# Performance work log

Measured on AMD Instinct MI355X. Metric: run time of the kernel, lower is better.

Reference implementation:

```python
import jax, jax.numpy as jnp
import numpy as np

B, D, LP, P = 64, 256, 64, 16
N = 256                     # linear1 output = number of graph nodes (= d_model for consistent reassembly)
F = LP * P                  # per-node feature dim = SAGEConv input_dim = 1024
HID = 512                   # hidden_channels
NODE_SLICES = {"A": (0, 128), "B": (128, 192), "C": (192, 256)}
# 6 cross edge types + 3 self-loop edge types (add_self_loops=True)
EDGE_TYPES = [("A", "B"), ("B", "A"), ("A", "C"), ("C", "A"), ("B", "C"), ("C", "B"),
              ("A", "A"), ("B", "B"), ("C", "C")]
E = len(EDGE_TYPES)


def setup_inputs() -> dict:
    ks = jax.random.split(jax.random.key(0), 8)
    s = lambda fan: 1.0 / np.sqrt(fan)
    return {
        "x": jax.random.normal(ks[0], (B, D, LP, P), jnp.float32),
        "W1": jax.random.normal(ks[1], (D, N), jnp.float32) * s(D),   # linear1
        "b1": jnp.zeros((N,), jnp.float32),
        "Wl": jax.random.normal(ks[2], (E, F, HID), jnp.float32) * s(F),  # SAGEConv lin_l (aggregated msgs)
        "bl": jnp.zeros((E, HID), jnp.float32),
        "Wr": jax.random.normal(ks[3], (E, F, HID), jnp.float32) * s(F),  # SAGEConv lin_r (root, no bias)
        "Wf": jax.random.normal(ks[4], (HID, F), jnp.float32) * s(HID),   # final_linear
        "bf": jnp.zeros((F,), jnp.float32),
        "W2": jax.random.normal(ks[5], (N, D), jnp.float32) * s(N),       # linear2
        "b2": jnp.zeros((D,), jnp.float32),
        "period": P,
    }


def reference(x, W1, b1, Wl, bl, Wr, Wf, bf, W2, b2, period):
    b = x.shape[0]
    # linear1 over channel dim: [B,D,LP,P] -> [B,N,LP,P]
    h = jnp.einsum('bdlp,dn->bnlp', x, W1) + b1[None, :, None, None]
    hf = h.reshape(b, N, -1)                                  # node features [B, N, F]
    xt = {t: hf[:, lo:hi] for t, (lo, hi) in NODE_SLICES.items()}
    # complete bipartite graph => scatter-mean over incoming edges == mean over all src nodes
    mu = {t: v.mean(axis=1) for t, v in xt.items()}           # [B, F]
    contribs = {t: [] for t in NODE_SLICES}
    for i, (s_t, d_t) in enumerate(EDGE_TYPES):
        # SAGEConv(mean): lin_l(aggr msgs) + lin_r(x_dst)
        c = (mu[s_t] @ Wl[i] + bl[i])[:, None, :] + jnp.einsum('bnf,fh->bnh', xt[d_t], Wr[i])
        contribs[d_t].append(c)
    outs = []
    for t in ("A", "B", "C"):
        o = jnp.mean(jnp.stack(contribs[t]), axis=0)          # HeteroConv aggr='mean' over edge types
        o = jax.nn.relu(o) @ Wf + bf                          # relu + final_linear -> [B, n_t, F]
        outs.append(o)
    out = jnp.concatenate(outs, axis=1)                       # [B, N, F] (A,B,C slices are contiguous)
    out = out.reshape(b, N, -1, period)                       # [B, N, LP, P]
    # linear2 over node/channel dim
    y = jnp.einsum('bnlp,nd->bdlp', out, W2) + b2[None, :, None, None]
    return y
```

## Files before the change

### kernel.cpp

```cpp
#include <hip/hip_runtime.h>

typedef unsigned short u16;
typedef __attribute__((ext_vector_type(8))) short bf16x8;
typedef __attribute__((ext_vector_type(4))) float f32x4;

constexpr int BB = 64;
constexpr int NN = 256;
constexpr int SS = 1024;
constexpr int FF = 1024;
constexpr int HH = 512;

__device__ const int d_eArr[3][3] = {{1, 3, 6}, {0, 5, 7}, {2, 4, 8}};
__device__ const int d_slotE[3][3] = {{2, 0, 0}, {0, 2, 1}, {1, 1, 2}};

__device__ __forceinline__ u16 f2bf(float f) {
    union { float f; unsigned u; } v; v.f = f;
    unsigned r = v.u + 0x7FFFu + ((v.u >> 16) & 1u);
    return (u16)(r >> 16);
}
__device__ __forceinline__ float bf2f(u16 h) {
    union { unsigned u; float f; } v; v.u = ((unsigned)h) << 16;
    return v.f;
}

typedef const __attribute__((address_space(1))) void gv_t;
typedef __attribute__((address_space(3))) void lv_t;
__device__ __forceinline__ void gl16(const void* g, void* l) {
    __builtin_amdgcn_global_load_lds((gv_t*)g, (lv_t*)l, 16, 0, 0);
}
__device__ __forceinline__ int swzv(int r) { return (r ^ (r >> 2)) & 3; }

template<int N> __device__ __forceinline__ void waitvm();
template<> __device__ __forceinline__ void waitvm<0>()  { asm volatile("s_waitcnt vmcnt(0)" ::: "memory"); }
template<> __device__ __forceinline__ void waitvm<2>()  { asm volatile("s_waitcnt vmcnt(2)" ::: "memory"); }
template<> __device__ __forceinline__ void waitvm<4>()  { asm volatile("s_waitcnt vmcnt(4)" ::: "memory"); }
template<> __device__ __forceinline__ void waitvm<6>()  { asm volatile("s_waitcnt vmcnt(6)" ::: "memory"); }
template<> __device__ __forceinline__ void waitvm<8>()  { asm volatile("s_waitcnt vmcnt(8)" ::: "memory"); }
template<> __device__ __forceinline__ void waitvm<12>() { asm volatile("s_waitcnt vmcnt(12)" ::: "memory"); }

__device__ __forceinline__ int g5row(int t, int g, int r) {
    if (t == 0) return (g << 8) + r;
    const int bp = (t == 1) ? (g - 64) : (g - 96);
    const int b  = (bp << 1) + (r >> 6);
    const int n  = ((t == 1) ? 128 : 192) + (r & 63);
    return (b << 8) + n;
}

__global__ __launch_bounds__(256)
void transpose_bf16(const float* __restrict__ in, u16* __restrict__ out, int R, int C) {
    __shared__ float tile[32][33];
    const int b = blockIdx.z;
    in  += (size_t)b * R * C;
    out += (size_t)b * R * C;
    const int c0 = blockIdx.x * 32, r0 = blockIdx.y * 32;
    const int x = threadIdx.x & 31, y = threadIdx.x >> 5;
#pragma unroll
    for (int k = 0; k < 4; ++k)
        tile[y + 8 * k][x] = in[(size_t)(r0 + y + 8 * k) * C + c0 + x];
    __syncthreads();
#pragma unroll
    for (int k = 0; k < 4; ++k)
        out[(size_t)(c0 + y + 8 * k) * R + r0 + x] = f2bf(tile[x][y + 8 * k]);
}

__device__ __forceinline__ void tr32(const float* __restrict__ in, u16* __restrict__ out,
                                     int R, int C, int bx, int by, float (*tile)[33]) {
    const int c0 = bx * 32, r0 = by * 32;
    const int x = threadIdx.x & 31, y = threadIdx.x >> 5;
#pragma unroll
    for (int k = 0; k < 4; ++k)
        tile[y + 8 * k][x] = in[(size_t)(r0 + y + 8 * k) * C + c0 + x];
    __syncthreads();
#pragma unroll
    for (int k = 0; k < 4; ++k)
        out[(size_t)(c0 + y + 8 * k) * R + r0 + x] = f2bf(tile[x][y + 8 * k]);
}

__global__ __launch_bounds__(256)
void prep_weights(const float* __restrict__ W1, const float* __restrict__ W2,
                  const float* __restrict__ Wf, const float* __restrict__ Wl,
                  const float* __restrict__ Wr, const float* __restrict__ bl,
                  u16* __restrict__ W1T, u16* __restrict__ W2T, u16* __restrict__ WfT,
                  u16* __restrict__ WlTc, u16* __restrict__ WsumT, float* __restrict__ blsum)
{
    __shared__ float tile[32][33];
    int id = blockIdx.x;
    if (id < 64) { tr32(W1, W1T, 256, 256, id & 7, id >> 3, tile); return; }
    id -= 64;
    if (id < 64) { tr32(W2, W2T, 256, 256, id & 7, id >> 3, tile); return; }
    id -= 64;
    if (id < 512) { tr32(Wf, WfT, 512, 1024, id & 31, id >> 5, tile); return; }
    id -= 512;
    if (id < 4608) {
        const int p = id >> 9, rem = id & 511;
        const int bx = rem & 15, by = rem >> 4;
        const int t = p / 3, ep = p % 3, e = d_eArr[t][ep];
        const int h0 = bx * 32, f0 = by * 32;
        const int x = threadIdx.x & 31, y = threadIdx.x >> 5;
        const float* src = Wl + (size_t)e * FF * HH;
#pragma unroll
        for (int k = 0; k < 4; ++k)
            tile[y + 8 * k][x] = src[(size_t)(f0 + y + 8 * k) * HH + h0 + x];
        __syncthreads();
        u16* dst = WlTc + (size_t)t * HH * 3072 + (size_t)ep * 1024;
#pragma unroll
        for (int k = 0; k < 4; ++k)
            dst[(size_t)(h0 + y + 8 * k) * 3072 + f0 + x] = f2bf(tile[x][y + 8 * k]);
        return;
    }
    id -= 4608;
    if (id < 1536) {
        const int t = id >> 9, rem = id & 511;
        const int bx = rem & 15, by = rem >> 4;
        const int h0 = bx * 32, f0 = by * 32;
        const int x = threadIdx.x & 31, y = threadIdx.x >> 5;
        const int e0 = d_eArr[t][0], e1 = d_eArr[t][1], e2 = d_eArr[t][2];
#pragma unroll
        for (int k = 0; k < 4; ++k) {
            const size_t off = (size_t)(f0 + y + 8 * k) * HH + h0 + x;
            float s = Wr[(size_t)e0 * FF * HH + off] + Wr[(size_t)e1 * FF * HH + off] +
                      Wr[(size_t)e2 * FF * HH + off];
            tile[y + 8 * k][x] = s * (1.f / 3.f);
        }
        __syncthreads();
        u16* dst = WsumT + (size_t)t * HH * FF;
#pragma unroll
        for (int k = 0; k < 4; ++k)
            dst[(size_t)(h0 + y + 8 * k) * FF + f0 + x] = f2bf(tile[x][y + 8 * k]);
        return;
    }
#pragma unroll
    for (int j = 0; j < 6; ++j) {
        const int idx = j * 256 + threadIdx.x;
        const int t = idx >> 9, hh = idx & 511;
        blsum[t * HH + hh] = bl[d_eArr[t][0] * HH + hh] + bl[d_eArr[t][1] * HH + hh] +
                             bl[d_eArr[t][2] * HH + hh];
    }
}

template<int BM, int BN, int KLEN, int EPI, int MODE>
__global__ __launch_bounds__(256, 2)
void gemm2(const u16* __restrict__ Abase, const u16* __restrict__ Bbase,
           void* __restrict__ Cbase, const float* __restrict__ aux1,
           const float* __restrict__ aux2, u16* __restrict__ muOut,
           long long sB, long long sC, int ldA, int ldB, int ldC)
{
    constexpr int WM = BM / 2, WN = BN / 2;
    constexpr int FM = WM / 16, FN = WN / 16;
    constexpr int NIA = (BM * 4) / 256, NIB = (BN * 4) / 256;
    constexpr int LPS = NIA + NIB;
    constexpr int BUFB = (BM + BN) * 64;
    constexpr int NT = KLEN / 32;
    static_assert(NT >= 3, "need >=3 K-steps");
    __shared__ __align__(16) unsigned char smem[3 * BUFB];

    const int tid = threadIdx.x, lane = tid & 63, wave = tid >> 6;
    const int wm = wave >> 1, wn = wave & 1;
    const int n0 = blockIdx.x * BN;

    int m0 = 0, b = 0, t = 0, g = 0;
    const u16* Ab; const u16* Bb;
    if constexpr (MODE == 0) {
        b  = blockIdx.z;
        m0 = blockIdx.y * BM;
        Ab = Abase + (size_t)m0 * ldA;
        Bb = Bbase + (size_t)b * sB + (size_t)n0 * ldB;
    } else if constexpr (MODE == 1) {
        g  = blockIdx.y;
        t  = (g < 64) ? 0 : (g < 96 ? 1 : 2);
        Ab = Abase;
        Bb = Bbase + (size_t)t * (HH * FF) + (size_t)n0 * ldB;
    } else {
        t  = blockIdx.z;
        const int k0 = blockIdx.y * KLEN;
        Ab = Abase + (size_t)t * 64 * ldA + k0;
        Bb = Bbase + (size_t)t * (HH * 3072) + (size_t)n0 * ldB + k0;
    }

    const u16* gAp[NIA]; const u16* gBp[NIB];
    int lAo[NIA], lBo[NIB];
#pragma unroll
    for (int i = 0; i < NIA; ++i) {
        const int c = i * 256 + tid, r = c >> 2, jl = c & 3;
        const int js = jl ^ swzv(r);
        size_t rowoff;
        if constexpr (MODE == 1) rowoff = (size_t)g5row(t, g, r) * FF;
        else                     rowoff = (size_t)r * ldA;
        gAp[i] = Ab + rowoff + js * 8;
        lAo[i] = c * 16;
    }
#pragma unroll
    for (int i = 0; i < NIB; ++i) {
        const int c = i * 256 + tid, r = c >> 2, jl = c & 3;
        const int js = jl ^ swzv(r);
        gBp[i] = Bb + (size_t)r * ldB + js * 8;
        lBo[i] = BM * 64 + c * 16;
    }
    const int q = lane >> 4;
    int rAo[FM], rBo[FN];
#pragma unroll
    for (int i = 0; i < FM; ++i) {
        const int r = wm * WM + i * 16 + (lane & 15);
        rAo[i] = (r * 4 + (q ^ swzv(r))) * 16;
    }
#pragma unroll
    for (int j = 0; j < FN; ++j) {
        const int r = wn * WN + j * 16 + (lane & 15);
        rBo[j] = BM * 64 + (r * 4 + (q ^ swzv(r))) * 16;
    }

    char* sm = (char*)smem;
    auto stage = [&](int bufo, int it) {
        const int kofs = it * 32;
#pragma unroll
        for (int i = 0; i < NIA; ++i)
            gl16(gAp[i] + kofs, sm + bufo + lAo[i]);
#pragma unroll
        for (int i = 0; i < NIB; ++i)
            gl16(gBp[i] + kofs, sm + bufo + lBo[i]);
    };

    const f32x4 zero4 = {0.f, 0.f, 0.f, 0.f};
    f32x4 acc[FM][FN];
#pragma unroll
    for (int i = 0; i < FM; ++i)
#pragma unroll
        for (int j = 0; j < FN; ++j) acc[i][j] = zero4;

    stage(0, 0);
    stage(BUFB, 1);
    stage(2 * BUFB, 2);

    int bufo = 0;
    for (int it = 0; it < NT; ++it) {
        if (it < NT - 2)       waitvm<2 * LPS>();
        else if (it == NT - 2) waitvm<LPS>();
        else                   waitvm<0>();
        __builtin_amdgcn_s_barrier();

        bf16x8 af[FM], bq[FN];
#pragma unroll
        for (int i = 0; i < FM; ++i) af[i] = *(const bf16x8*)(sm + bufo + rAo[i]);
#pragma unroll
        for (int j = 0; j < FN; ++j) bq[j] = *(const bf16x8*)(sm + bufo + rBo[j]);
        asm volatile("s_waitcnt lgkmcnt(0)" ::: "memory");
        __builtin_amdgcn_sched_barrier(0);

        __builtin_amdgcn_s_setprio(1);
#pragma unroll
        for (int i = 0; i < FM; ++i)
#pragma unroll
            for (int j = 0; j < FN; ++j)
                acc[i][j] = __builtin_amdgcn_mfma_f32_16x16x32_bf16(af[i], bq[j], acc[i][j], 0, 0, 0);
        __builtin_amdgcn_s_setprio(0);

        __builtin_amdgcn_s_barrier();
        if (it + 3 < NT) stage(bufo, it + 3);
        bufo = (bufo == 2 * BUFB) ? 0 : bufo + BUFB;
    }

    const int q4   = q << 2;
    const int colb = n0 + wn * WN + (lane & 15);
    if constexpr (EPI == 0) {
        u16* C = (u16*)Cbase + (size_t)b * sC;
#pragma unroll
        for (int i = 0; i < FM; ++i)
#pragma unroll
            for (int rr = 0; rr < 4; ++rr) {
                const int row = m0 + wm * WM + i * 16 + q4 + rr;
                const float bias = aux1[row];
#pragma unroll
                for (int j = 0; j < FN; ++j)
                    C[(size_t)row * ldC + colb + j * 16] = f2bf(acc[i][j][rr] + bias);
            }
    } else if constexpr (EPI == 3) {
        float* C = (float*)Cbase + (size_t)b * sC;
#pragma unroll
        for (int i = 0; i < FM; ++i)
#pragma unroll
            for (int rr = 0; rr < 4; ++rr) {
                const int row = m0 + wm * WM + i * 16 + q4 + rr;
                const float bias = aux1[row];
#pragma unroll
                for (int j = 0; j < FN; ++j)
                    C[(size_t)row * ldC + colb + j * 16] = acc[i][j][rr] + bias;
            }
    } else if constexpr (EPI == 1) {
        float* C = (float*)Cbase + (size_t)blockIdx.y * 98304 + (size_t)t * (64 * HH);
#pragma unroll
        for (int i = 0; i < FM; ++i)
#pragma unroll
            for (int rr = 0; rr < 4; ++rr) {
                const int row = wm * WM + i * 16 + q4 + rr;
#pragma unroll
                for (int j = 0; j < FN; ++j)
                    C[(size_t)row * HH + colb + j * 16] = acc[i][j][rr];
            }
    } else if constexpr (EPI == 2) {
        u16* C = (u16*)Cbase;
        const int bb = (t == 0) ? g : ((((t == 1) ? (g - 64) : (g - 96)) << 1) + wm);
        float bet[FN];
#pragma unroll
        for (int j = 0; j < FN; ++j) {
            const int col = colb + j * 16;
            float s = 0.f;
#pragma unroll
            for (int ks = 0; ks < 8; ++ks)
                s += aux1[(size_t)ks * 98304 + (size_t)((t << 6) + bb) * HH + col];
            bet[j] = (s + aux2[t * HH + col]) * (1.f / 3.f);
        }
#pragma unroll
        for (int i = 0; i < FM; ++i)
#pragma unroll
            for (int rr = 0; rr < 4; ++rr) {
                const int rl = wm * WM + i * 16 + q4 + rr;
                const int glob = g5row(t, g, rl);
#pragma unroll
                for (int j = 0; j < FN; ++j) {
                    const float v = acc[i][j][rr] + bet[j];
                    C[(size_t)glob * ldC + colb + j * 16] = f2bf(fmaxf(v, 0.f));
                }
            }
    } else {
        u16* C = (u16*)Cbase + (size_t)b * sC;
        float t0[FN], t1[FN];
#pragma unroll
        for (int j = 0; j < FN; ++j) { t0[j] = 0.f; t1[j] = 0.f; }
#pragma unroll
        for (int i = 0; i < FM; ++i)
#pragma unroll
            for (int rr = 0; rr < 4; ++rr) {
                const int row = m0 + wm * WM + i * 16 + q4 + rr;
                const float bias = aux1[row];
#pragma unroll
                for (int j = 0; j < FN; ++j) {
                    const float hv = acc[i][j][rr] + bias;
                    C[(size_t)row * ldC + colb + j * 16] = f2bf(hv);
                    if (wm == 0)            t0[j] += hv;
                    else if (i < FM / 2)    t0[j] += hv;
                    else                    t1[j] += hv;
                }
            }
#pragma unroll
        for (int j = 0; j < FN; ++j) {
            t0[j] += __shfl_xor(t0[j], 16, 64);
            t0[j] += __shfl_xor(t0[j], 32, 64);
            t1[j] += __shfl_xor(t1[j], 16, 64);
            t1[j] += __shfl_xor(t1[j], 32, 64);
        }
        if (lane < 16) {
#pragma unroll
            for (int j = 0; j < FN; ++j) {
                const int col = colb + j * 16;
                if (wm == 0) {
                    const u16 v = f2bf(t0[j] * (1.f / 128.f));
#pragma unroll
                    for (int tt = 0; tt < 3; ++tt)
                        muOut[((size_t)tt * BB + b) * 3072 + (size_t)d_slotE[0][tt] * 1024 + col] = v;
                } else {
                    const u16 vB = f2bf(t0[j] * (1.f / 64.f));
                    const u16 vC = f2bf(t1[j] * (1.f / 64.f));
#pragma unroll
                    for (int tt = 0; tt < 3; ++tt) {
                        muOut[((size_t)tt * BB + b) * 3072 + (size_t)d_slotE[1][tt] * 1024 + col] = vB;
                        muOut[((size_t)tt * BB + b) * 3072 + (size_t)d_slotE[2][tt] * 1024 + col] = vC;
                    }
                }
            }
        }
    }
}

extern "C" void kernel_launch(void* const* d_in, const int* in_sizes, int n_in,
                              void* d_out, int out_size, void* d_ws, size_t ws_size,
                              hipStream_t stream) {
    const float* x  = (const float*)d_in[0];
    const float* W1 = (const float*)d_in[1];
    const float* b1 = (const float*)d_in[2];
    const float* Wl = (const float*)d_in[3];
    const float* bl = (const float*)d_in[4];
    const float* Wr = (const float*)d_in[5];
    const float* Wf = (const float*)d_in[6];
    const float* bf = (const float*)d_in[7];
    const float* W2 = (const float*)d_in[8];
    const float* b2 = (const float*)d_in[9];
    float* y = (float*)d_out;

    u16* wsS   = (u16*)d_ws;
    u16* xT    = wsS;
    u16* h     = wsS + 16777216;
    u16* r     = wsS + 33554432;
    u16* W1T   = wsS + 41943040;
    u16* W2T   = wsS + 42008576;
    u16* WfT   = wsS + 42074112;
    u16* WsumT = wsS + 42598400;
    u16* WlTc  = wsS + 44171264;
    u16* muCat = wsS + 48889856;
    float* blsum = (float*)(wsS + 49479680);
    float* tmp8 = (float*)xT;
    u16* outT = xT;

    prep_weights<<<dim3(6785), 256, 0, stream>>>(W1, W2, Wf, Wl, Wr, bl,
                                                 W1T, W2T, WfT, WlTc, WsumT, blsum);
    transpose_bf16<<<dim3(32, 8, 64), 256, 0, stream>>>(x, xT, 256, 1024);

    gemm2<256, 128, 256, 4, 0><<<dim3(8, 1, 64), 256, 0, stream>>>(
        W1T, xT, h, b1, nullptr, muCat, 262144, 262144, 256, 256, 1024);
    gemm2<64, 64, 384, 1, 2><<<dim3(8, 8, 3), 256, 0, stream>>>(
        muCat, WlTc, tmp8, nullptr, nullptr, nullptr, 0, 0, 3072, 3072, 512);
    gemm2<128, 128, 1024, 2, 1><<<dim3(4, 128, 1), 256, 0, stream>>>(
        h, WsumT, r, tmp8, blsum, nullptr, 0, 0, 1024, 1024, 512);
    gemm2<256, 128, 512, 0, 0><<<dim3(2, 4, 64), 256, 0, stream>>>(
        WfT, r, outT, bf, nullptr, nullptr, 131072, 262144, 512, 512, 256);
    gemm2<256, 128, 256, 3, 0><<<dim3(8, 1, 64), 256, 0, stream>>>(
        W2T, outT, y, b2, nullptr, nullptr, 262144, 262144, 256, 256, 1024);
}
```

Before: 133.2 us.

## Stage GEMM epilogues through LDS for vectorized stores and remap block order

```diff
diff --git a/kernel.cpp b/kernel.cpp
--- a/kernel.cpp
+++ b/kernel.cpp
@@ -81,7 +81,8 @@
                   const float* __restrict__ Wf, const float* __restrict__ Wl,
                   const float* __restrict__ Wr, const float* __restrict__ bl,
                   u16* __restrict__ W1T, u16* __restrict__ W2T, u16* __restrict__ WfT,
-                  u16* __restrict__ WlTc, u16* __restrict__ WsumT, float* __restrict__ blsum)
+                  u16* __restrict__ WlTc, u16* __restrict__ WsumT,
+                  float* __restrict__ blsum)
 {
     __shared__ float tile[32][33];
     int id = blockIdx.x;
@@ -138,7 +139,7 @@
     }
 }
 
-template<int BM, int BN, int KLEN, int EPI, int MODE>
+template<int BM, int BN, int KLEN, int EPI, int MODE, int NX>
 __global__ __launch_bounds__(256, 2)
 void gemm2(const u16* __restrict__ Abase, const u16* __restrict__ Bbase,
            void* __restrict__ Cbase, const float* __restrict__ aux1,
@@ -153,25 +154,31 @@
     constexpr int NT = KLEN / 32;
     static_assert(NT >= 3, "need >=3 K-steps");
     __shared__ __align__(16) unsigned char smem[3 * BUFB];
+    char* sm = (char*)smem;
 
     const int tid = threadIdx.x, lane = tid & 63, wave = tid >> 6;
     const int wm = wave >> 1, wn = wave & 1;
-    const int n0 = blockIdx.x * BN;
-
-    int m0 = 0, b = 0, t = 0, g = 0;
-    const u16* Ab; const u16* Bb;
+
+    int n0 = 0, m0 = 0, b = 0, t = 0, g = 0;
+    const u16* Ab = nullptr; const u16* Bb = nullptr;
     if constexpr (MODE == 0) {
-        b  = blockIdx.z;
-        m0 = blockIdx.y * BM;
+        const int id = blockIdx.x;
+        b  = id & 63;
+        const int kx = id >> 6;
+        n0 = (kx % NX) * BN;
+        m0 = (kx / NX) * BM;
         Ab = Abase + (size_t)m0 * ldA;
         Bb = Bbase + (size_t)b * sB + (size_t)n0 * ldB;
     } else if constexpr (MODE == 1) {
-        g  = blockIdx.y;
+        const int id = blockIdx.x;
+        g  = id & 127;
+        n0 = (id >> 7) * BN;
         t  = (g < 64) ? 0 : (g < 96 ? 1 : 2);
         Ab = Abase;
         Bb = Bbase + (size_t)t * (HH * FF) + (size_t)n0 * ldB;
     } else {
         t  = blockIdx.z;
+        n0 = blockIdx.x * BN;
         const int k0 = blockIdx.y * KLEN;
         Ab = Abase + (size_t)t * 64 * ldA + k0;
         Bb = Bbase + (size_t)t * (HH * 3072) + (size_t)n0 * ldB + k0;
@@ -192,8 +199,7 @@
 #pragma unroll
     for (int i = 0; i < NIB; ++i) {
         const int c = i * 256 + tid, r = c >> 2, jl = c & 3;
-        const int js = jl ^ swzv(r);
-        gBp[i] = Bb + (size_t)r * ldB + js * 8;
+        gBp[i] = Bb + (size_t)r * ldB + (jl ^ swzv(r)) * 8;
         lBo[i] = BM * 64 + c * 16;
     }
     const int q = lane >> 4;
@@ -209,15 +215,12 @@
         rBo[j] = BM * 64 + (r * 4 + (q ^ swzv(r))) * 16;
     }
 
-    char* sm = (char*)smem;
     auto stage = [&](int bufo, int it) {
         const int kofs = it * 32;
 #pragma unroll
-        for (int i = 0; i < NIA; ++i)
-            gl16(gAp[i] + kofs, sm + bufo + lAo[i]);
-#pragma unroll
-        for (int i = 0; i < NIB; ++i)
-            gl16(gBp[i] + kofs, sm + bufo + lBo[i]);
+        for (int i = 0; i < NIA; ++i) gl16(gAp[i] + kofs, sm + bufo + lAo[i]);
+#pragma unroll
+        for (int i = 0; i < NIB; ++i) gl16(gBp[i] + kofs, sm + bufo + lBo[i]);
     };
 
     const f32x4 zero4 = {0.f, 0.f, 0.f, 0.f};
@@ -259,34 +262,12 @@
         bufo = (bufo == 2 * BUFB) ? 0 : bufo + BUFB;
     }
 
-    const int q4   = q << 2;
-    const int colb = n0 + wn * WN + (lane & 15);
-    if constexpr (EPI == 0) {
-        u16* C = (u16*)Cbase + (size_t)b * sC;
-#pragma unroll
-        for (int i = 0; i < FM; ++i)
-#pragma unroll
-            for (int rr = 0; rr < 4; ++rr) {
-                const int row = m0 + wm * WM + i * 16 + q4 + rr;
-                const float bias = aux1[row];
-#pragma unroll
-                for (int j = 0; j < FN; ++j)
-                    C[(size_t)row * ldC + colb + j * 16] = f2bf(acc[i][j][rr] + bias);
-            }
-    } else if constexpr (EPI == 3) {
-        float* C = (float*)Cbase + (size_t)b * sC;
-#pragma unroll
-        for (int i = 0; i < FM; ++i)
-#pragma unroll
-            for (int rr = 0; rr < 4; ++rr) {
-                const int row = m0 + wm * WM + i * 16 + q4 + rr;
-                const float bias = aux1[row];
-#pragma unroll
-                for (int j = 0; j < FN; ++j)
-                    C[(size_t)row * ldC + colb + j * 16] = acc[i][j][rr] + bias;
-            }
-    } else if constexpr (EPI == 1) {
+    const int q4 = q << 2;
+    constexpr int BNP = BN + 8;
+
+    if constexpr (EPI == 1) {
         float* C = (float*)Cbase + (size_t)blockIdx.y * 98304 + (size_t)t * (64 * HH);
+        const int colb = n0 + wn * WN + (lane & 15);
 #pragma unroll
         for (int i = 0; i < FM; ++i)
 #pragma unroll
@@ -296,77 +277,121 @@
                 for (int j = 0; j < FN; ++j)
                     C[(size_t)row * HH + colb + j * 16] = acc[i][j][rr];
             }
-    } else if constexpr (EPI == 2) {
-        u16* C = (u16*)Cbase;
-        const int bb = (t == 0) ? g : ((((t == 1) ? (g - 64) : (g - 96)) << 1) + wm);
+    } else if constexpr (EPI == 0 || EPI == 4 || EPI == 2) {
+        u16* lds = (u16*)sm;
+        const int lcb = wn * WN + (lane & 15);
+        float t0[FN], t1[FN];
+        if constexpr (EPI == 4) {
+#pragma unroll
+            for (int j = 0; j < FN; ++j) { t0[j] = 0.f; t1[j] = 0.f; }
+        }
         float bet[FN];
-#pragma unroll
-        for (int j = 0; j < FN; ++j) {
-            const int col = colb + j * 16;
-            float s = 0.f;
-#pragma unroll
-            for (int ks = 0; ks < 8; ++ks)
-                s += aux1[(size_t)ks * 98304 + (size_t)((t << 6) + bb) * HH + col];
-            bet[j] = (s + aux2[t * HH + col]) * (1.f / 3.f);
+        if constexpr (EPI == 2) {
+            const int bb = (t == 0) ? g : ((((t == 1) ? (g - 64) : (g - 96)) << 1) + wm);
+#pragma unroll
+            for (int j = 0; j < FN; ++j) {
+                const int col = n0 + lcb + j * 16;
+                float s = aux2[t * HH + col];
+#pragma unroll
+                for (int ks = 0; ks < 8; ++ks)
+                    s += aux1[(size_t)ks * 98304 + (size_t)((t << 6) + bb) * HH + col];
+                bet[j] = s * (1.f / 3.f);
+            }
         }
 #pragma unroll
         for (int i = 0; i < FM; ++i)
 #pragma unroll
             for (int rr = 0; rr < 4; ++rr) {
-                const int rl = wm * WM + i * 16 + q4 + rr;
-                const int glob = g5row(t, g, rl);
+                const int lrow = wm * WM + i * 16 + q4 + rr;
+                float bias = 0.f;
+                if constexpr (EPI == 0 || EPI == 4) bias = aux1[m0 + lrow];
 #pragma unroll
                 for (int j = 0; j < FN; ++j) {
-                    const float v = acc[i][j][rr] + bet[j];
-                    C[(size_t)glob * ldC + colb + j * 16] = f2bf(fmaxf(v, 0.f));
-                }
-            }
-    } else {
-        u16* C = (u16*)Cbase + (size_t)b * sC;
-        float t0[FN], t1[FN];
-#pragma unroll
-        for (int j = 0; j < FN; ++j) { t0[j] = 0.f; t1[j] = 0.f; }
-#pragma unroll
-        for (int i = 0; i < FM; ++i)
-#pragma unroll
-            for (int rr = 0; rr < 4; ++rr) {
-                const int row = m0 + wm * WM + i * 16 + q4 + rr;
-                const float bias = aux1[row];
-#pragma unroll
-                for (int j = 0; j < FN; ++j) {
-                    const float hv = acc[i][j][rr] + bias;
-                    C[(size_t)row * ldC + colb + j * 16] = f2bf(hv);
-                    if (wm == 0)            t0[j] += hv;
-                    else if (i < FM / 2)    t0[j] += hv;
-                    else                    t1[j] += hv;
-                }
-            }
-#pragma unroll
-        for (int j = 0; j < FN; ++j) {
-            t0[j] += __shfl_xor(t0[j], 16, 64);
-            t0[j] += __shfl_xor(t0[j], 32, 64);
-            t1[j] += __shfl_xor(t1[j], 16, 64);
-            t1[j] += __shfl_xor(t1[j], 32, 64);
-        }
-        if (lane < 16) {
-#pragma unroll
-            for (int j = 0; j < FN; ++j) {
-                const int col = colb + j * 16;
-                if (wm == 0) {
-                    const u16 v = f2bf(t0[j] * (1.f / 128.f));
-#pragma unroll
-                    for (int tt = 0; tt < 3; ++tt)
-                        muOut[((size_t)tt * BB + b) * 3072 + (size_t)d_slotE[0][tt] * 1024 + col] = v;
-                } else {
-                    const u16 vB = f2bf(t0[j] * (1.f / 64.f));
-                    const u16 vC = f2bf(t1[j] * (1.f / 64.f));
-#pragma unroll
-                    for (int tt = 0; tt < 3; ++tt) {
-                        muOut[((size_t)tt * BB + b) * 3072 + (size_t)d_slotE[1][tt] * 1024 + col] = vB;
-                        muOut[((size_t)tt * BB + b) * 3072 + (size_t)d_slotE[2][tt] * 1024 + col] = vC;
+                    float v = acc[i][j][rr] + ((EPI == 2) ? bet[j] : bias);
+                    if constexpr (EPI == 2) v = fmaxf(v, 0.f);
+                    lds[lrow * BNP + lcb + j * 16] = f2bf(v);
+                    if constexpr (EPI == 4) {
+                        const float hv = v;
+                        if (wm == 0)            t0[j] += hv;
+                        else if (i < FM / 2)    t0[j] += hv;
+                        else                    t1[j] += hv;
                     }
                 }
             }
+        __syncthreads();
+        {
+            u16* Cg;
+            if constexpr (EPI == 2) Cg = (u16*)Cbase;
+            else                    Cg = (u16*)Cbase + (size_t)b * sC;
+            constexpr int CH = (BM * BN) / (256 * 8);
+#pragma unroll
+            for (int c = 0; c < CH; ++c) {
+                const int e   = (c * 256 + tid) * 8;
+                const int row = e / BN, col = e % BN;
+                const bf16x8 v = *(const bf16x8*)&lds[row * BNP + col];
+                size_t goff;
+                if constexpr (EPI == 2) goff = (size_t)g5row(t, g, row) * ldC + n0 + col;
+                else                    goff = (size_t)(m0 + row) * ldC + n0 + col;
+                *(bf16x8*)(Cg + goff) = v;
+            }
+        }
+        if constexpr (EPI == 4) {
+#pragma unroll
+            for (int j = 0; j < FN; ++j) {
+                t0[j] += __shfl_xor(t0[j], 16, 64);
+                t0[j] += __shfl_xor(t0[j], 32, 64);
+                t1[j] += __shfl_xor(t1[j], 16, 64);
+                t1[j] += __shfl_xor(t1[j], 32, 64);
+            }
+            if (lane < 16) {
+#pragma unroll
+                for (int j = 0; j < FN; ++j) {
+                    const int col = n0 + lcb + j * 16;
+                    if (wm == 0) {
+                        const u16 v = f2bf(t0[j] * (1.f / 128.f));
+#pragma unroll
+                        for (int tt = 0; tt < 3; ++tt)
+                            muOut[((size_t)tt * BB + b) * 3072 + (size_t)d_slotE[0][tt] * 1024 + col] = v;
+                    } else {
+                        const u16 vB = f2bf(t0[j] * (1.f / 64.f));
+                        const u16 vC = f2bf(t1[j] * (1.f / 64.f));
+#pragma unroll
+                        for (int tt = 0; tt < 3; ++tt) {
+                            muOut[((size_t)tt * BB + b) * 3072 + (size_t)d_slotE[1][tt] * 1024 + col] = vB;
+                            muOut[((size_t)tt * BB + b) * 3072 + (size_t)d_slotE[2][tt] * 1024 + col] = vC;
+                        }
+                    }
+                }
+            }
+        }
+    } else {
+        float* lf = (float*)sm;
+        float* Cg = (float*)Cbase + (size_t)b * sC;
+        const int lcb = wn * WN + (lane & 15);
+#pragma unroll
+        for (int half = 0; half < 2; ++half) {
+            if (wm == half) {
+#pragma unroll
+                for (int i = 0; i < FM; ++i)
+#pragma unroll
+                    for (int rr = 0; rr < 4; ++rr) {
+                        const int lrow = i * 16 + q4 + rr;
+                        const float bias = aux1[m0 + half * WM + lrow];
+#pragma unroll
+                        for (int j = 0; j < FN; ++j)
+                            lf[lrow * BNP + lcb + j * 16] = acc[i][j][rr] + bias;
+                    }
+            }
+            __syncthreads();
+            constexpr int CH = (WM * BN) / (256 * 4);
+#pragma unroll
+            for (int c = 0; c < CH; ++c) {
+                const int e   = (c * 256 + tid) * 4;
+                const int row = e / BN, col = e % BN;
+                const f32x4 v = *(const f32x4*)&lf[row * BNP + col];
+                *(f32x4*)(Cg + (size_t)(m0 + half * WM + row) * ldC + n0 + col) = v;
+            }
+            __syncthreads();
         }
     }
 }
@@ -396,22 +421,22 @@
     u16* WsumT = wsS + 42598400;
     u16* WlTc  = wsS + 44171264;
     u16* muCat = wsS + 48889856;
-    float* blsum = (float*)(wsS + 49479680);
-    float* tmp8 = (float*)xT;
+    float* tmp8  = (float*)(wsS + 49479680);
+    float* blsum = tmp8 + 786432;
     u16* outT = xT;
 
     prep_weights<<<dim3(6785), 256, 0, stream>>>(W1, W2, Wf, Wl, Wr, bl,
                                                  W1T, W2T, WfT, WlTc, WsumT, blsum);
     transpose_bf16<<<dim3(32, 8, 64), 256, 0, stream>>>(x, xT, 256, 1024);
 
-    gemm2<256, 128, 256, 4, 0><<<dim3(8, 1, 64), 256, 0, stream>>>(
+    gemm2<256, 128, 256, 4, 0, 8><<<dim3(512), 256, 0, stream>>>(
         W1T, xT, h, b1, nullptr, muCat, 262144, 262144, 256, 256, 1024);
-    gemm2<64, 64, 384, 1, 2><<<dim3(8, 8, 3), 256, 0, stream>>>(
+    gemm2<64, 64, 384, 1, 2, 1><<<dim3(8, 8, 3), 256, 0, stream>>>(
         muCat, WlTc, tmp8, nullptr, nullptr, nullptr, 0, 0, 3072, 3072, 512);
-    gemm2<128, 128, 1024, 2, 1><<<dim3(4, 128, 1), 256, 0, stream>>>(
+    gemm2<128, 128, 1024, 2, 1, 4><<<dim3(512), 256, 0, stream>>>(
         h, WsumT, r, tmp8, blsum, nullptr, 0, 0, 1024, 1024, 512);
-    gemm2<256, 128, 512, 0, 0><<<dim3(2, 4, 64), 256, 0, stream>>>(
+    gemm2<256, 128, 512, 0, 0, 2><<<dim3(512), 256, 0, stream>>>(
         WfT, r, outT, bf, nullptr, nullptr, 131072, 262144, 512, 512, 256);
-    gemm2<256, 128, 256, 3, 0><<<dim3(8, 1, 64), 256, 0, stream>>>(
+    gemm2<256, 128, 256, 3, 0, 8><<<dim3(512), 256, 0, stream>>>(
         W2T, outT, y, b2, nullptr, nullptr, 262144, 262144, 256, 256, 1024);
 }
```

Result: no change. 130.7 us (-1.9%).
